# Kernel optimization log

Measured on AMD Instinct MI355X. Metric: run time of the kernel, lower is better.

Reference implementation:

```python
import jax, jax.numpy as jnp
import numpy as np

DIM = 512
WINDOW = 8
HEADS = 16
HEAD_DIM = DIM // HEADS
SIGMA = 0.39
B = 2048
N = WINDOW * WINDOW


def gaussian_kernel(window_size, sigma):
    """Row-normalised Gaussian attention mask K_sigma (M^2 x M^2)."""
    c = jnp.arange(window_size, dtype=jnp.float32)
    gy, gx = jnp.meshgrid(c, c, indexing='ij')
    pos = jnp.stack([gy.flatten(), gx.flatten()], -1)  # [M^2, 2]
    diff = pos[None, :, :] - pos[:, None, :]           # [M^2, M^2, 2]
    K = jnp.exp(-(diff ** 2).sum(-1) / (2.0 * sigma ** 2))
    return K / K.sum(-1, keepdims=True)


def setup_inputs() -> dict:
    key = jax.random.key(0)
    k1, k2, k3, k4, k5 = jax.random.split(key, 5)
    x = jax.random.normal(k1, (B, N, DIM), dtype=jnp.float32)
    # spectral_norm at inference is just a fixed scaling of the weight; we
    # model the (already-normalised) weights as plain dense params.
    w_qkv = jax.random.normal(k2, (DIM, 3 * DIM), dtype=jnp.float32) * (DIM ** -0.5)
    b_qkv = jax.random.normal(k3, (3 * DIM,), dtype=jnp.float32) * 0.02
    w_proj = jax.random.normal(k4, (DIM, DIM), dtype=jnp.float32) * (DIM ** -0.5)
    b_proj = jax.random.normal(k5, (DIM,), dtype=jnp.float32) * 0.02
    return {"x": x, "w_qkv": w_qkv, "b_qkv": b_qkv, "w_proj": w_proj, "b_proj": b_proj}


def reference(x, w_qkv, b_qkv, w_proj, b_proj):
    Bb, Nn, C = x.shape
    scale = HEAD_DIM ** -0.5
    qkv = (x @ w_qkv + b_qkv).reshape(Bb, Nn, 3, HEADS, HEAD_DIM)
    qkv = jnp.transpose(qkv, (2, 0, 3, 1, 4))  # [3, B, H, N, D]
    q, k, v = qkv[0], qkv[1], qkv[2]
    attn = jnp.einsum('bhnd,bhmd->bhnm', q, k) * scale  # [B, H, N, N]
    K_s = gaussian_kernel(WINDOW, SIGMA)                 # [N, N]
    attn = jax.nn.softmax(attn * K_s, axis=-1)
    out = jnp.einsum('bhnm,bhmd->bhnd', attn, v)         # [B, H, N, D]
    out = jnp.transpose(out, (0, 2, 1, 3)).reshape(Bb, Nn, C)
    return out @ w_proj + b_proj
```

## Files before the change

kernel.cpp:

```cpp
#include <hip/hip_runtime.h>
#include <hip/hip_bf16.h>
#include <stdint.h>

typedef __bf16 bf16;
typedef __bf16 bf16x8 __attribute__((ext_vector_type(8)));
typedef float f32x4 __attribute__((ext_vector_type(4)));
typedef unsigned short u16t;
typedef unsigned int u32t;

#define MFMA16(a, b, c) __builtin_amdgcn_mfma_f32_16x16x32_bf16((a), (b), (c), 0, 0, 0)

typedef const void __attribute__((address_space(1))) cg_void;
typedef void __attribute__((address_space(3))) lds_void;
#define GLL16(g, l) __builtin_amdgcn_global_load_lds((cg_void*)(g), (lds_void*)(l), 16, 0, 0)
#define VWAIT(n) asm volatile("s_waitcnt vmcnt(" #n ")" ::: "memory")

#define OFF_FLAG   0
#define OFF_BQKV   256
#define OFF_BPROJ  6400
#define OFF_WQKVT  8448
#define OFF_WPROJT 1581312
#define OFF_QKV    2105600
#define OFF_XB     404758784



__global__ __launch_bounds__(256) void k_detect(const u16t* x, u32t* flag) {
    __shared__ int cnt;
    if (threadIdx.x == 0) cnt = 0;
    __syncthreads();
    u16t h = x[threadIdx.x * 2];
    int e = (h >> 7) & 0xFF;
    int ok = (h == 0) || (e >= 100 && e <= 134);
    atomicAdd(&cnt, ok);
    __syncthreads();
    if (threadIdx.x == 0) flag[0] = (cnt >= 200) ? 1u : 0u;
}

__global__ __launch_bounds__(256) void k_cvt(const float* x, bf16* xb, const u32t* flagp) {
    if (flagp[0]) return;
    const size_t TOT = (size_t)131072 * 512;
    size_t i = (size_t)(blockIdx.x * 256 + threadIdx.x) * 8;
    const size_t stride = (size_t)gridDim.x * 256 * 8;
    for (; i < TOT; i += stride) {
        float4 v0 = *(const float4*)(x + i);
        float4 v1 = *(const float4*)(x + i + 4);
        bf16x8 h;
        h[0] = (bf16)v0.x; h[1] = (bf16)v0.y; h[2] = (bf16)v0.z; h[3] = (bf16)v0.w;
        h[4] = (bf16)v1.x; h[5] = (bf16)v1.y; h[6] = (bf16)v1.z; h[7] = (bf16)v1.w;
        *(bf16x8*)(xb + i) = h;
    }
}

template <int N, bool PERM>
__global__ __launch_bounds__(256) void k_trans(const void* W, bf16* Wt, const u32t* flagp) {
    __shared__ float T[64][65];
    const int isbf = (int)flagp[0];
    const int n0 = blockIdx.x * 64, k0 = blockIdx.y * 64;
    const int t = threadIdx.x;
    const int lc = t & 63, lr = t >> 6;
#pragma unroll
    for (int rr = 0; rr < 16; ++rr) {
        int row = rr * 4 + lr;
        int col = n0 + lc;
        int srcc = col;
        if (PERM) {
            int h = col / 96, r = col % 96;
            srcc = (r >> 5) * 512 + h * 32 + (r & 31);
        }
        size_t g = (size_t)(k0 + row) * N + srcc;
        float v = isbf ? (float)((const bf16*)W)[g] : ((const float*)W)[g];
        T[row][lc] = v;
    }
    __syncthreads();
#pragma unroll
    for (int rr = 0; rr < 16; ++rr) {
        int row = rr * 4 + lr;
        Wt[(size_t)(n0 + row) * 512 + k0 + lc] = (bf16)T[lc][row];
    }
}

__global__ __launch_bounds__(256) void k_bias(const void* b_qkv, const void* b_proj,
                                              const u32t* flagp, char* ws) {
    float* bq = (float*)(ws + OFF_BQKV);
    float* bp = (float*)(ws + OFF_BPROJ);
    const int isbf = (int)flagp[0];
    int gid = blockIdx.x * 256 + threadIdx.x;
    if (gid < 1536) {
        int h = gid / 96, r = gid % 96;
        int src = (r >> 5) * 512 + h * 32 + (r & 31);
        bq[gid] = isbf ? (float)((const bf16*)b_qkv)[src] : ((const float*)b_qkv)[src];
    } else if (gid < 2048) {
        int o = gid - 1536;
        bp[o] = isbf ? (float)((const bf16*)b_proj)[o] : ((const float*)b_proj)[o];
    }
}

template <int NTOT>
__global__ __launch_bounds__(512, 2) void k_gemm(const void* Ax, const bf16* Axb, const bf16* Bt,
                                                 const float* bias, void* Cp,
                                                 const u32t* flagp, int omode) {
    __shared__ __align__(16) u16t As[2 * 8192];
    __shared__ __align__(16) u16t Bs[2 * 8192];
    constexpr int NBN = NTOT / 256;
    const int isbf = (int)flagp[0];
    const int out_bf16 = (omode == 1) || isbf;
    const bf16* Ab = isbf ? (const bf16*)Ax : Axb;

    const int t = threadIdx.x;
    const int w = t >> 6, lane = t & 63;
    const int ln = lane & 15, qd = lane >> 4;
    const int wm = w >> 2, wn = w & 3;

    const int flat = blockIdx.x;
    const int xcd = flat & 7, slot = flat >> 3;
    const int n_idx = slot % NBN, grp = slot / NBN;
    const int m0 = (grp * 8 + xcd) * 256;
    const int n0 = n_idx * 256;

    const int l8 = lane >> 3, p8 = lane & 7;
    const int cl = p8 ^ l8;
    const int tok_l = 2 * l8 + (cl >> 2);
    const int koff = (cl & 3) * 8;

    u32t asrc[2], bsrc[2];
    int adst[2], bdst[2];
#pragma unroll
    for (int s = 0; s < 2; ++s) {
        int RsA = s * 32 + (w >> 2) * 64 + (w & 3) * 8;
        asrc[s] = (u32t)(m0 + 2 * RsA + tok_l) * 512 + koff;
        adst[s] = RsA * 64;
        int RsB = s * 16 + (w >> 1) * 32 + (w & 1) * 8;
        bsrc[s] = (u32t)(n0 + 2 * RsB + tok_l) * 512 + koff;
        bdst[s] = RsB * 64;
    }

    const int fph = (((ln & 1) * 4 + qd) ^ ((ln >> 1) & 7)) * 8;
    int abase[4], bbase[2];
#pragma unroll
    for (int i = 0; i < 4; ++i) abase[i] = (wm * 64 + i * 8 + (ln >> 1)) * 64 + fph;
#pragma unroll
    for (int j = 0; j < 2; ++j) bbase[j] = (wn * 32 + j * 8 + (ln >> 1)) * 64 + fph;

    f32x4 acc[8][4];
    f32x4 zero = {0.f, 0.f, 0.f, 0.f};
#pragma unroll
    for (int i = 0; i < 8; ++i)
#pragma unroll
        for (int j = 0; j < 4; ++j) acc[i][j] = zero;

    auto stageA = [&](int s, int buf, int kt) {
        GLL16(Ab + asrc[s] + kt * 32, &As[buf * 8192 + adst[s]]);
    };
    auto stageB = [&](int s, int buf, int kt) {
        GLL16(Bt + bsrc[s] + kt * 32, &Bs[buf * 8192 + bdst[s]]);
    };

#define PHX(BUF, QM, QN, LOADA, STG, WAITOP)                                    \
    {                                                                           \
        if (LOADA) {                                                            \
            _Pragma("unroll") for (int i = 0; i < 4; ++i)                       \
                af[i] = *(const bf16x8*)(const void*)                           \
                    &As[(BUF) * 8192 + (QM) * 2048 + abase[i]];                 \
        }                                                                       \
        _Pragma("unroll") for (int j = 0; j < 2; ++j)                           \
            bv[j] = *(const bf16x8*)(const void*)                               \
                &Bs[(BUF) * 8192 + (QN) * 1024 + bbase[j]];                     \
        STG;                                                                    \
        WAITOP;                                                                 \
        __builtin_amdgcn_s_barrier();                                           \
        __builtin_amdgcn_s_setprio(1);                                          \
        _Pragma("unroll") for (int i = 0; i < 4; ++i)                           \
            _Pragma("unroll") for (int j = 0; j < 2; ++j)                       \
                acc[(QM) * 4 + i][(QN) * 2 + j] =                               \
                    MFMA16(af[i], bv[j], acc[(QM) * 4 + i][(QN) * 2 + j]);      \
        __builtin_amdgcn_s_setprio(0);                                          \
        __builtin_amdgcn_s_barrier();                                           \
    }

    stageA(0, 0, 0);
    stageB(0, 0, 0);
    stageB(1, 0, 0);
    stageA(1, 0, 0);
    VWAIT(2);
    __builtin_amdgcn_s_barrier();

    for (int kt = 0; kt < 16; ++kt) {
        const int buf = kt & 1, nb = buf ^ 1, k1 = kt + 1;
        bf16x8 af[4], bv[2];
        if (kt < 15) {
            PHX(buf, 0, 0, 1, stageA(0, nb, k1), VWAIT(2));
            PHX(buf, 0, 1, 0, stageB(0, nb, k1), VWAIT(2));
            PHX(buf, 1, 0, 1, stageB(1, nb, k1), (void)0);
            PHX(buf, 1, 1, 0, stageA(1, nb, k1), VWAIT(2));
        } else {
            PHX(buf, 0, 0, 1, (void)0, VWAIT(1));
            PHX(buf, 0, 1, 0, (void)0, VWAIT(0));
            PHX(buf, 1, 0, 1, (void)0, (void)0);
            PHX(buf, 1, 1, 0, (void)0, (void)0);
        }
    }
#undef PHX

    float bj[4];
#pragma unroll
    for (int j = 0; j < 4; ++j) bj[j] = bias[n0 + wn * 64 + j * 16 + ln];

    if (out_bf16) {
        bf16* C = (bf16*)Cp;
#pragma unroll
        for (int i = 0; i < 8; ++i)
#pragma unroll
            for (int j = 0; j < 4; ++j)
#pragma unroll
                for (int rr = 0; rr < 4; ++rr) {
                    size_t row = (size_t)m0 + wm * 128 + i * 16 + qd * 4 + rr;
                    int col = n0 + wn * 64 + j * 16 + ln;
                    C[row * NTOT + col] = (bf16)(acc[i][j][rr] + bj[j]);
                }
    } else {
        float* C = (float*)Cp;
#pragma unroll
        for (int i = 0; i < 8; ++i)
#pragma unroll
            for (int j = 0; j < 4; ++j)
#pragma unroll
                for (int rr = 0; rr < 4; ++rr) {
                    size_t row = (size_t)m0 + wm * 128 + i * 16 + qd * 4 + rr;
                    int col = n0 + wn * 64 + j * 16 + ln;
                    C[row * NTOT + col] = acc[i][j][rr] + bj[j];
                }
    }
}

__global__ __launch_bounds__(256, 3) void k_fuse5(const void* Ax, const bf16* Axb,
                                                  const bf16* Bt, const float* bias,
                                                  bf16* attnout, const u32t* flagp) {
    __shared__ __align__(16) u16t pool[26624];
    const int isbf = (int)flagp[0];
    const bf16* Ab = isbf ? (const bf16*)Ax : Axb;

    const int t = threadIdx.x;
    const int w = t >> 6, lane = t & 63;
    const int ln = lane & 15, qd = lane >> 4, q8 = qd * 8;
    const int wm = w >> 1, wn = w & 1;

    const int flat = blockIdx.x;
    const int xcd = flat & 7, slot = flat >> 3;
    const int n_idx = slot & 7, mgrp = slot >> 3;
    const int blkm = mgrp * 8 + xcd;
    const int m0 = blkm * 128;
    const int n0 = n_idx * 192;
    const int win = blkm * 2 + wm;
    const int g = n_idx * 2 + wn;

    const int l8 = lane >> 3, p8 = lane & 7;
    const int cl = p8 ^ l8;
    const int tok_l = 2 * l8 + (cl >> 2);
    const int koff = (cl & 3) * 8;

    u32t asrc[2];
    int adst[2];
#pragma unroll
    for (int q = 0; q < 2; ++q) {
        int Rs = w * 16 + q * 8;
        asrc[q] = (u32t)(m0 + 2 * Rs + tok_l) * 512 + koff;
        adst[q] = Rs * 64;
    }
    u32t bsrc[3];
    int bdst[3];
#pragma unroll
    for (int r = 0; r < 3; ++r) {
        int Rs = (w & 1) * 48 + r * 16 + (w >> 1) * 8;
        bsrc[r] = (u32t)(n0 + 2 * Rs + tok_l) * 512 + koff;
        bdst[r] = Rs * 64;
    }

    const int fph = (((ln & 1) * 4 + qd) ^ ((ln >> 1) & 7)) * 8;
    int afo[4], bfo[6];
#pragma unroll
    for (int i = 0; i < 4; ++i) afo[i] = (wm * 32 + i * 8 + (ln >> 1)) * 64 + fph;
#pragma unroll
    for (int j = 0; j < 6; ++j) bfo[j] = (wn * 48 + j * 8 + (ln >> 1)) * 64 + fph;

    f32x4 acc[4][6];
    f32x4 zero = {0.f, 0.f, 0.f, 0.f};
#pragma unroll
    for (int i = 0; i < 4; ++i)
#pragma unroll
        for (int j = 0; j < 6; ++j) acc[i][j] = zero;

    auto ST_A = [&](int buf, int kt) {
#pragma unroll
        for (int q = 0; q < 2; ++q)
            GLL16(Ab + asrc[q] + kt * 32, &pool[buf * 4096 + adst[q]]);
    };
    auto ST_R = [&](int r, int buf, int kt) {
        GLL16(Bt + bsrc[r] + kt * 32, &pool[8192 + buf * 6144 + bdst[r]]);
    };

    ST_A(0, 0);
    ST_R(0, 0, 0);
    ST_R(1, 0, 0);
    ST_R(2, 0, 0);
    VWAIT(2);
    __builtin_amdgcn_s_barrier();

    for (int kt = 0; kt < 16; ++kt) {
        const int buf = kt & 1, nb = buf ^ 1;
        const u16t* Abuf = &pool[buf * 4096];
        const u16t* Bbuf = &pool[8192 + buf * 6144];
        bf16x8 af[4], bv[2];

#pragma unroll
        for (int i = 0; i < 4; ++i)
            af[i] = *(const bf16x8*)(const void*)&Abuf[afo[i]];
        bv[0] = *(const bf16x8*)(const void*)&Bbuf[bfo[0]];
        bv[1] = *(const bf16x8*)(const void*)&Bbuf[bfo[1]];
        if (kt < 15) { ST_A(nb, kt + 1); ST_R(0, nb, kt + 1); VWAIT(4); }
        else VWAIT(1);
        __builtin_amdgcn_s_barrier();
        __builtin_amdgcn_s_setprio(1);
#pragma unroll
        for (int i = 0; i < 4; ++i) {
            acc[i][0] = MFMA16(af[i], bv[0], acc[i][0]);
            acc[i][1] = MFMA16(af[i], bv[1], acc[i][1]);
        }
        __builtin_amdgcn_s_setprio(0);
        __builtin_amdgcn_s_barrier();

        bv[0] = *(const bf16x8*)(const void*)&Bbuf[bfo[2]];
        bv[1] = *(const bf16x8*)(const void*)&Bbuf[bfo[3]];
        if (kt < 15) { ST_R(1, nb, kt + 1); VWAIT(4); }
        else VWAIT(0);
        __builtin_amdgcn_s_barrier();
        __builtin_amdgcn_s_setprio(1);
#pragma unroll
        for (int i = 0; i < 4; ++i) {
            acc[i][2] = MFMA16(af[i], bv[0], acc[i][2]);
            acc[i][3] = MFMA16(af[i], bv[1], acc[i][3]);
        }
        __builtin_amdgcn_s_setprio(0);
        __builtin_amdgcn_s_barrier();

        bv[0] = *(const bf16x8*)(const void*)&Bbuf[bfo[4]];
        bv[1] = *(const bf16x8*)(const void*)&Bbuf[bfo[5]];
        if (kt < 15) { ST_R(2, nb, kt + 1); VWAIT(2); }
        __builtin_amdgcn_s_barrier();
        __builtin_amdgcn_s_setprio(1);
#pragma unroll
        for (int i = 0; i < 4; ++i) {
            acc[i][4] = MFMA16(af[i], bv[0], acc[i][4]);
            acc[i][5] = MFMA16(af[i], bv[1], acc[i][5]);
        }
        __builtin_amdgcn_s_setprio(0);
        __builtin_amdgcn_s_barrier();
    }

    float bj[6];
#pragma unroll
    for (int j = 0; j < 6; ++j) bj[j] = bias[g * 96 + j * 16 + ln];
    u16t* pw = &pool[w * 6656];
#pragma unroll
    for (int i = 0; i < 4; ++i)
#pragma unroll
        for (int j = 0; j < 6; ++j) {
            int part = j >> 1;
            int d = (j & 1) * 16 + ln;
#pragma unroll
            for (int rr = 0; rr < 4; ++rr) {
                int tok = i * 16 + qd * 4 + rr;
                bf16 val = (bf16)(acc[i][j][rr] + bj[j]);
                int idx;
                if (part == 2)
                    idx = 4608 + tok * 32 +
                          (((d >> 3) ^ (((tok >> 3) ^ tok) & 3)) << 3) + (d & 7);
                else
                    idx = part * 2048 + tok * 32 +
                          (((d >> 3) ^ ((tok >> 1) & 3)) << 3) + (d & 7);
                *(bf16*)&pw[idx] = val;
            }
        }

    {
        const int hcol = g * 32;
        const int qswz = (qd ^ ((ln >> 1) & 3)) * 8;

        bf16x8 aq[4], bk[4];
#pragma unroll
        for (int i = 0; i < 4; ++i)
            aq[i] = *(const bf16x8*)(const void*)&pw[(i * 16 + ln) * 32 + qswz];
#pragma unroll
        for (int j = 0; j < 4; ++j)
            bk[j] = *(const bf16x8*)(const void*)&pw[2048 + (j * 16 + ln) * 32 + qswz];

        f32x4 zro = {0.f, 0.f, 0.f, 0.f};
        f32x4 s[4][4];
#pragma unroll
        for (int i = 0; i < 4; ++i)
#pragma unroll
            for (int j = 0; j < 4; ++j) s[i][j] = MFMA16(aq[i], bk[j], zro);

        const float INV2S2 = 3.28731097961867f;
        {
            int c = lane & 7;
            float S1 = 0.f;
#pragma unroll
            for (int c2 = 0; c2 < 8; ++c2) {
                int dd = c - c2;
                S1 += __expf(-(float)(dd * dd) * INV2S2);
            }
            float invS1 = 1.0f / S1;
            const int ymb = ln >> 3, xm = ln & 7, yq = qd >> 1, xq = (qd & 1) * 4;
            float FY[4][4], FX[4];
#pragma unroll
            for (int i = 0; i < 4; ++i) {
                int yn = 2 * i + yq;
                float gg = __shfl(invS1, yn, 64);
#pragma unroll
                for (int j = 0; j < 4; ++j) {
                    int dy = yn - (2 * j + ymb);
                    FY[i][j] = __expf(-(float)(dy * dy) * INV2S2) * gg;
                }
            }
#pragma unroll
            for (int rr = 0; rr < 4; ++rr) {
                int xn = xq + rr;
                int dx = xn - xm;
                FX[rr] = __expf(-(float)(dx * dx) * INV2S2) * __shfl(invS1, xn, 64);
            }

            const float SCALE = 0.17677669529663687f;
#pragma unroll
            for (int i = 0; i < 4; ++i)
#pragma unroll
                for (int rr = 0; rr < 4; ++rr) {
                    float lj[4];
                    float mx = -1e30f;
#pragma unroll
                    for (int j = 0; j < 4; ++j) {
                        lj[j] = s[i][j][rr] * SCALE * FY[i][j] * FX[rr];
                        mx = fmaxf(mx, lj[j]);
                    }
                    mx = fmaxf(mx, __shfl_xor(mx, 1));
                    mx = fmaxf(mx, __shfl_xor(mx, 2));
                    mx = fmaxf(mx, __shfl_xor(mx, 4));
                    mx = fmaxf(mx, __shfl_xor(mx, 8));
                    float sum = 0.f;
#pragma unroll
                    for (int j = 0; j < 4; ++j) {
                        lj[j] = __expf(lj[j] - mx);
                        sum += lj[j];
                    }
                    sum += __shfl_xor(sum, 1);
                    sum += __shfl_xor(sum, 2);
                    sum += __shfl_xor(sum, 4);
                    sum += __shfl_xor(sum, 8);
                    float inv = 1.0f / sum;
                    int n = i * 16 + qd * 4 + rr;
#pragma unroll
                    for (int j = 0; j < 4; ++j) {
                        bf16 pv = (bf16)(lj[j] * inv);
                        *(bf16*)&pw[n * 72 + j * 16 + ln] = pv;
                    }
                }
        }

        f32x4 o[4][2];
#pragma unroll
        for (int i = 0; i < 4; ++i) {
            o[i][0] = zro;
            o[i][1] = zro;
        }
#pragma unroll
        for (int kc = 0; kc < 64; kc += 32) {
            bf16x8 bv2[2];
#pragma unroll
            for (int j2 = 0; j2 < 2; ++j2) {
                int cc = j2 * 2 + (ln >> 3);
#pragma unroll
                for (int jj = 0; jj < 8; ++jj) {
                    int rv = kc + q8 + jj;
                    bv2[j2][jj] = *(const bf16*)&pw[4608 + rv * 32 +
                                                   ((cc ^ (((rv >> 3) ^ rv) & 3)) << 3) + (ln & 7)];
                }
            }
#pragma unroll
            for (int i = 0; i < 4; ++i) {
                bf16x8 ap = *(const bf16x8*)(const void*)&pw[(i * 16 + ln) * 72 + kc + q8];
#pragma unroll
                for (int j2 = 0; j2 < 2; ++j2) o[i][j2] = MFMA16(ap, bv2[j2], o[i][j2]);
            }
        }
#pragma unroll
        for (int i = 0; i < 4; ++i)
#pragma unroll
            for (int j2 = 0; j2 < 2; ++j2)
#pragma unroll
                for (int rr = 0; rr < 4; ++rr)
                    attnout[((size_t)win * 64 + i * 16 + qd * 4 + rr) * 512 +
                            hcol + j2 * 16 + ln] = (bf16)(o[i][j2][rr]);
    }
}

extern "C" void kernel_launch(void* const* d_in, const int* in_sizes, int n_in,
                              void* d_out, int out_size, void* d_ws, size_t ws_size,
                              hipStream_t stream) {
    const void* x = d_in[0];
    const void* w_qkv = d_in[1];
    const void* b_qkv = d_in[2];
    const void* w_proj = d_in[3];
    const void* b_proj = d_in[4];
    char* ws = (char*)d_ws;
    u32t* flag = (u32t*)(ws + OFF_FLAG);
    bf16* wqkvT = (bf16*)(ws + OFF_WQKVT);
    bf16* wprojT = (bf16*)(ws + OFF_WPROJT);
    float* bq = (float*)(ws + OFF_BQKV);
    float* bp = (float*)(ws + OFF_BPROJ);
    bf16* attnout = (bf16*)(ws + OFF_QKV);
    bf16* xb = (bf16*)(ws + OFF_XB);

    k_detect<<<1, 256, 0, stream>>>((const u16t*)x, flag);
    k_cvt<<<2048, 256, 0, stream>>>((const float*)x, xb, flag);
    k_trans<1536, true><<<dim3(24, 8), 256, 0, stream>>>(w_qkv, wqkvT, flag);
    k_trans<512, false><<<dim3(8, 8), 256, 0, stream>>>(w_proj, wprojT, flag);
    k_bias<<<8, 256, 0, stream>>>(b_qkv, b_proj, flag, ws);
    k_fuse5<<<8192, 256, 0, stream>>>(x, xb, wqkvT, bq, attnout, flag);
    k_gemm<512><<<1024, 512, 0, stream>>>((const void*)attnout, attnout, wprojT, bp, d_out, flag, 2);
}
```

Before: 864.2 us.

## Halve output projection GEMM M-tile to 128 rows and restructure pipeline

The projection GEMM now computes 128x256 output tiles instead of 256x256, launching twice as many blocks with half the A-tile LDS. The launch bound goes to four blocks per SM. The k-loop is rebuilt into two MFMA phases per step with a deeper A prefetch (two k-steps ahead) and split B staging. This aims to raise occupancy and improve load balance across CUs, at the cost of less B-tile reuse per block and more total global traffic for weights.

```diff
diff --git a/kernel.cpp b/kernel.cpp
--- a/kernel.cpp
+++ b/kernel.cpp
@@ -97,10 +97,10 @@
 }
 
 template <int NTOT>
-__global__ __launch_bounds__(512, 2) void k_gemm(const void* Ax, const bf16* Axb, const bf16* Bt,
+__global__ __launch_bounds__(512, 4) void k_gemm(const void* Ax, const bf16* Axb, const bf16* Bt,
                                                  const float* bias, void* Cp,
                                                  const u32t* flagp, int omode) {
-    __shared__ __align__(16) u16t As[2 * 8192];
+    __shared__ __align__(16) u16t As[2 * 4096];
     __shared__ __align__(16) u16t Bs[2 * 8192];
     constexpr int NBN = NTOT / 256;
     const int isbf = (int)flagp[0];
@@ -114,8 +114,8 @@
 
     const int flat = blockIdx.x;
     const int xcd = flat & 7, slot = flat >> 3;
-    const int n_idx = slot % NBN, grp = slot / NBN;
-    const int m0 = (grp * 8 + xcd) * 256;
+    const int n_idx = slot % NBN, mgrp = slot / NBN;
+    const int m0 = (mgrp * 8 + xcd) * 128;
     const int n0 = n_idx * 256;
 
     const int l8 = lane >> 3, p8 = lane & 7;
@@ -123,84 +123,79 @@
     const int tok_l = 2 * l8 + (cl >> 2);
     const int koff = (cl & 3) * 8;
 
-    u32t asrc[2], bsrc[2];
-    int adst[2], bdst[2];
-#pragma unroll
-    for (int s = 0; s < 2; ++s) {
-        int RsA = s * 32 + (w >> 2) * 64 + (w & 3) * 8;
-        asrc[s] = (u32t)(m0 + 2 * RsA + tok_l) * 512 + koff;
-        adst[s] = RsA * 64;
-        int RsB = s * 16 + (w >> 1) * 32 + (w & 1) * 8;
-        bsrc[s] = (u32t)(n0 + 2 * RsB + tok_l) * 512 + koff;
-        bdst[s] = RsB * 64;
-    }
+    const int RsA = w * 8;
+    const u32t asrc = (u32t)(m0 + 2 * RsA + tok_l) * 512 + koff;
+    const int adst = RsA * 64;
+    const int RsB0 = (w & 3) * 32 + (w >> 2) * 8;
+    const u32t bsrc0 = (u32t)(n0 + 2 * RsB0 + tok_l) * 512 + koff;
+    const int bdst0 = RsB0 * 64;
+    const u32t bsrc1 = bsrc0 + 32 * 512;
+    const int bdst1 = bdst0 + 16 * 64;
 
     const int fph = (((ln & 1) * 4 + qd) ^ ((ln >> 1) & 7)) * 8;
-    int abase[4], bbase[2];
-#pragma unroll
-    for (int i = 0; i < 4; ++i) abase[i] = (wm * 64 + i * 8 + (ln >> 1)) * 64 + fph;
-#pragma unroll
-    for (int j = 0; j < 2; ++j) bbase[j] = (wn * 32 + j * 8 + (ln >> 1)) * 64 + fph;
-
-    f32x4 acc[8][4];
+    int abase[4], bbase[4];
+#pragma unroll
+    for (int i = 0; i < 4; ++i) abase[i] = (wm * 32 + i * 8 + (ln >> 1)) * 64 + fph;
+#pragma unroll
+    for (int j = 0; j < 4; ++j) bbase[j] = (wn * 32 + j * 8 + (ln >> 1)) * 64 + fph;
+
+    f32x4 acc[4][4];
     f32x4 zero = {0.f, 0.f, 0.f, 0.f};
 #pragma unroll
-    for (int i = 0; i < 8; ++i)
+    for (int i = 0; i < 4; ++i)
 #pragma unroll
         for (int j = 0; j < 4; ++j) acc[i][j] = zero;
 
-    auto stageA = [&](int s, int buf, int kt) {
-        GLL16(Ab + asrc[s] + kt * 32, &As[buf * 8192 + adst[s]]);
-    };
-    auto stageB = [&](int s, int buf, int kt) {
-        GLL16(Bt + bsrc[s] + kt * 32, &Bs[buf * 8192 + bdst[s]]);
-    };
-
-#define PHX(BUF, QM, QN, LOADA, STG, WAITOP)                                    \
-    {                                                                           \
-        if (LOADA) {                                                            \
-            _Pragma("unroll") for (int i = 0; i < 4; ++i)                       \
-                af[i] = *(const bf16x8*)(const void*)                           \
-                    &As[(BUF) * 8192 + (QM) * 2048 + abase[i]];                 \
-        }                                                                       \
-        _Pragma("unroll") for (int j = 0; j < 2; ++j)                           \
-            bv[j] = *(const bf16x8*)(const void*)                               \
-                &Bs[(BUF) * 8192 + (QN) * 1024 + bbase[j]];                     \
-        STG;                                                                    \
-        WAITOP;                                                                 \
-        __builtin_amdgcn_s_barrier();                                           \
-        __builtin_amdgcn_s_setprio(1);                                          \
-        _Pragma("unroll") for (int i = 0; i < 4; ++i)                           \
-            _Pragma("unroll") for (int j = 0; j < 2; ++j)                       \
-                acc[(QM) * 4 + i][(QN) * 2 + j] =                               \
-                    MFMA16(af[i], bv[j], acc[(QM) * 4 + i][(QN) * 2 + j]);      \
-        __builtin_amdgcn_s_setprio(0);                                          \
-        __builtin_amdgcn_s_barrier();                                           \
-    }
-
-    stageA(0, 0, 0);
-    stageB(0, 0, 0);
-    stageB(1, 0, 0);
-    stageA(1, 0, 0);
+    auto stA = [&](int buf, int kt) { GLL16(Ab + asrc + kt * 32, &As[buf * 4096 + adst]); };
+    auto stB0 = [&](int buf, int kt) { GLL16(Bt + bsrc0 + kt * 32, &Bs[buf * 8192 + bdst0]); };
+    auto stB1 = [&](int buf, int kt) { GLL16(Bt + bsrc1 + kt * 32, &Bs[buf * 8192 + bdst1]); };
+
+    stA(0, 0);
+    stB0(0, 0);
+    stB1(0, 0);
+    stA(1, 1);
     VWAIT(2);
     __builtin_amdgcn_s_barrier();
 
     for (int kt = 0; kt < 16; ++kt) {
-        const int buf = kt & 1, nb = buf ^ 1, k1 = kt + 1;
+        const int buf = kt & 1, nb = buf ^ 1;
         bf16x8 af[4], bv[2];
+
+#pragma unroll
+        for (int i = 0; i < 4; ++i)
+            af[i] = *(const bf16x8*)(const void*)&As[buf * 4096 + abase[i]];
+        bv[0] = *(const bf16x8*)(const void*)&Bs[buf * 8192 + bbase[0]];
+        bv[1] = *(const bf16x8*)(const void*)&Bs[buf * 8192 + bbase[1]];
+        if (kt < 15) { stB0(nb, kt + 1); VWAIT(2); }
+        else VWAIT(0);
+        __builtin_amdgcn_s_barrier();
+        __builtin_amdgcn_s_setprio(1);
+#pragma unroll
+        for (int i = 0; i < 4; ++i) {
+            acc[i][0] = MFMA16(af[i], bv[0], acc[i][0]);
+            acc[i][1] = MFMA16(af[i], bv[1], acc[i][1]);
+        }
+        __builtin_amdgcn_s_setprio(0);
+        __builtin_amdgcn_s_barrier();
+
+        bv[0] = *(const bf16x8*)(const void*)&Bs[buf * 8192 + bbase[2]];
+        bv[1] = *(const bf16x8*)(const void*)&Bs[buf * 8192 + bbase[3]];
         if (kt < 15) {
-            PHX(buf, 0, 0, 1, stageA(0, nb, k1), VWAIT(2));
-            PHX(buf, 0, 1, 0, stageB(0, nb, k1), VWAIT(2));
-            PHX(buf, 1, 0, 1, stageB(1, nb, k1), (void)0);
-            PHX(buf, 1, 1, 0, stageA(1, nb, k1), VWAIT(2));
-        } else {
-            PHX(buf, 0, 0, 1, (void)0, VWAIT(1));
-            PHX(buf, 0, 1, 0, (void)0, VWAIT(0));
-            PHX(buf, 1, 0, 1, (void)0, (void)0);
-            PHX(buf, 1, 1, 0, (void)0, (void)0);
-        }
-    }
-#undef PHX
+            stB1(nb, kt + 1);
+            if (kt < 14) stA(buf, kt + 2);
+            if (kt < 14) VWAIT(2);
+            else VWAIT(1);
+        }
+        __builtin_amdgcn_s_barrier();
+        __builtin_amdgcn_s_setprio(1);
+#pragma unroll
+        for (int i = 0; i < 4; ++i) {
+            acc[i][2] = MFMA16(af[i], bv[0], acc[i][2]);
+            acc[i][3] = MFMA16(af[i], bv[1], acc[i][3]);
+        }
+        __builtin_amdgcn_s_setprio(0);
+        __builtin_amdgcn_s_barrier();
+    }
 
     float bj[4];
 #pragma unroll
@@ -209,24 +204,24 @@
     if (out_bf16) {
         bf16* C = (bf16*)Cp;
 #pragma unroll
-        for (int i = 0; i < 8; ++i)
+        for (int i = 0; i < 4; ++i)
 #pragma unroll
             for (int j = 0; j < 4; ++j)
 #pragma unroll
                 for (int rr = 0; rr < 4; ++rr) {
-                    size_t row = (size_t)m0 + wm * 128 + i * 16 + qd * 4 + rr;
+                    size_t row = (size_t)m0 + wm * 64 + i * 16 + qd * 4 + rr;
                     int col = n0 + wn * 64 + j * 16 + ln;
                     C[row * NTOT + col] = (bf16)(acc[i][j][rr] + bj[j]);
                 }
     } else {
         float* C = (float*)Cp;
 #pragma unroll
-        for (int i = 0; i < 8; ++i)
+        for (int i = 0; i < 4; ++i)
 #pragma unroll
             for (int j = 0; j < 4; ++j)
 #pragma unroll
                 for (int rr = 0; rr < 4; ++rr) {
-                    size_t row = (size_t)m0 + wm * 128 + i * 16 + qd * 4 + rr;
+                    size_t row = (size_t)m0 + wm * 64 + i * 16 + qd * 4 + rr;
                     int col = n0 + wn * 64 + j * 16 + ln;
                     C[row * NTOT + col] = acc[i][j][rr] + bj[j];
                 }
@@ -526,5 +521,5 @@
     k_trans<512, false><<<dim3(8, 8), 256, 0, stream>>>(w_proj, wprojT, flag);
     k_bias<<<8, 256, 0, stream>>>(b_qkv, b_proj, flag, ws);
     k_fuse5<<<8192, 256, 0, stream>>>(x, xb, wqkvT, bq, attnout, flag);
-    k_gemm<512><<<1024, 512, 0, stream>>>((const void*)attnout, attnout, wprojT, bp, d_out, flag, 2);
-}
+    k_gemm<512><<<2048, 512, 0, stream>>>((const void*)attnout, attnout, wprojT, bp, d_out, flag, 2);
+}
```

New measurement: 838.0 us. -3.0%, faster.
